# Kernel tuning notes

Measured on AMD Instinct MI355X. Metric: run time of the kernel, lower is better.

The kernel has to match this reference:

```python
import jax, jax.numpy as jnp
import numpy as np
from jax import lax

EPS = 1e-5
NBIT = 127.0  # 8-bit symmetric: 2^(8-1)-1

def ste_round(x):
    return x + lax.stop_gradient(jnp.round(x) - x)

def quant_act(x, rng_max):
    # symmetric fake-quant of activations with learned per-cluster range
    s = rng_max / NBIT
    xq = jnp.clip(ste_round(x / s), -NBIT, NBIT) * s
    return xq, s

def fold_bn(w, gamma, beta, mean, var):
    std = jnp.sqrt(var + EPS)
    scale = gamma / std
    w_f = w * scale[:, None, None, None]
    b_f = beta - mean * scale
    return w_f, b_f

def quant_weight(w):
    # per-output-channel symmetric quant
    s = jnp.max(jnp.abs(w), axis=(1, 2, 3), keepdims=True) / NBIT
    wq = jnp.clip(ste_round(w / s), -NBIT, NBIT) * s
    return wq, s.reshape(-1)

def conv(x, w, stride=1, groups=1, pad=0):
    return lax.conv_general_dilated(
        x, w, window_strides=(stride, stride),
        padding=((pad, pad), (pad, pad)),
        dimension_numbers=('NCHW', 'OIHW', 'NCHW'),
        feature_group_count=groups)

def setup_inputs() -> dict:
    key = jax.random.key(0)
    ks = jax.random.split(key, 24)
    B, Cin, H, W = 64, 96, 28, 28
    Cmid, Cout, NC = 576, 96, 4
    d = {}
    d['x'] = jax.random.normal(ks[0], (B, Cin, H, W), dtype=jnp.float32)
    # conv1: 1x1 expansion
    d['w1'] = jax.random.normal(ks[1], (Cmid, Cin, 1, 1), jnp.float32) * 0.1
    d['g1'] = jax.random.uniform(ks[2], (Cmid,), minval=0.5, maxval=1.5)
    d['b1'] = jax.random.normal(ks[3], (Cmid,)) * 0.1
    d['m1'] = jax.random.normal(ks[4], (Cmid,)) * 0.1
    d['v1'] = jax.random.uniform(ks[5], (Cmid,), minval=0.5, maxval=1.5)
    # conv2: 3x3 depthwise
    d['w2'] = jax.random.normal(ks[6], (Cmid, 1, 3, 3), jnp.float32) * 0.1
    d['g2'] = jax.random.uniform(ks[7], (Cmid,), minval=0.5, maxval=1.5)
    d['b2'] = jax.random.normal(ks[8], (Cmid,)) * 0.1
    d['m2'] = jax.random.normal(ks[9], (Cmid,)) * 0.1
    d['v2'] = jax.random.uniform(ks[10], (Cmid,), minval=0.5, maxval=1.5)
    # conv3: 1x1 projection
    d['w3'] = jax.random.normal(ks[11], (Cout, Cmid, 1, 1), jnp.float32) * 0.1
    d['g3'] = jax.random.uniform(ks[12], (Cout,), minval=0.5, maxval=1.5)
    d['b3'] = jax.random.normal(ks[13], (Cout,)) * 0.1
    d['m3'] = jax.random.normal(ks[14], (Cout,)) * 0.1
    d['v3'] = jax.random.uniform(ks[15], (Cout,), minval=0.5, maxval=1.5)
    # per-cluster learned activation ranges for the 4 QuantAct modules
    d['r0'] = jax.random.uniform(ks[16], (NC,), minval=2.0, maxval=8.0)
    d['r1'] = jax.random.uniform(ks[17], (NC,), minval=2.0, maxval=8.0)
    d['r2'] = jax.random.uniform(ks[18], (NC,), minval=2.0, maxval=8.0)
    d['r3'] = jax.random.uniform(ks[19], (NC,), minval=2.0, maxval=8.0)
    d['cluster'] = 2
    return d

def reference(x, w1, g1, b1, m1, v1, w2, g2, b2, m2, v2,
              w3, g3, b3, m3, v3, r0, r1, r2, r3, cluster):
    identity = x  # residual path (in==out, stride==1)
    # QuantAct -> conv1 (BN-folded, per-channel quant) -> ReLU6
    xq, s0 = quant_act(x, r0[cluster])
    w1f, bf1 = fold_bn(w1, g1, b1, m1, v1)
    w1q, ws1 = quant_weight(w1f)
    y = conv(xq, w1q) + bf1[None, :, None, None]
    y = jnp.clip(y, 0.0, 6.0)
    # QuantAct1 -> depthwise conv2 -> ReLU6
    yq, s1 = quant_act(y, r1[cluster])
    w2f, bf2 = fold_bn(w2, g2, b2, m2, v2)
    w2q, ws2 = quant_weight(w2f)
    y = conv(yq, w2q, stride=1, groups=w2.shape[0], pad=1) + bf2[None, :, None, None]
    y = jnp.clip(y, 0.0, 6.0)
    # QuantAct2 -> conv3 projection
    yq, s2 = quant_act(y, r2[cluster])
    w3f, bf3 = fold_bn(w3, g3, b3, m3, v3)
    w3q, ws3 = quant_weight(w3f)
    y = conv(yq, w3q) + bf3[None, :, None, None]
    # residual add, then int32 requant
    y = y + identity
    out, s3 = quant_act(y, r3[cluster])
    return out, s3
```

## Files before the change

### kernel.cpp

```cpp
#include <hip/hip_runtime.h>
#include <cstdint>
#include <cstddef>

typedef int   v4i __attribute__((ext_vector_type(4)));
typedef float v4f __attribute__((ext_vector_type(4)));
typedef unsigned int u32;

constexpr int B_   = 64;
constexpr int CIN  = 96;
constexpr int P_   = 784;
constexpr int CMID = 576;
constexpr int COUT = 96;
constexpr int NOUT = B_ * COUT * P_;
constexpr float NBITF = 127.0f;
constexpr float EPSF  = 1e-5f;
constexpr float MAGICF = 12582912.0f;
constexpr int   BIASI  = 0x4B400000;

constexpr int XB4 = 13 * 8 * 64;
constexpr int YB4 = 13 * 36 * 64;

__device__ __forceinline__ int dot3(u32 a, u32 w, int acc) {
#if __has_builtin(__builtin_amdgcn_sdot4)
    return __builtin_amdgcn_sdot4((int)a, (int)w, acc, false);
#else
    return acc + (int)(signed char)(a)        * (int)(signed char)(w)
               + (int)(signed char)(a >> 8)   * (int)(signed char)(w >> 8)
               + (int)(signed char)(a >> 16)  * (int)(signed char)(w >> 16);
#endif
}

__device__ __forceinline__ void tr4(u32 S0, u32 S1, u32 S2, u32 S3, u32 O[4]) {
    u32 u01 = __builtin_amdgcn_perm(S1, S0, 0x05010400u);
    u32 u23 = __builtin_amdgcn_perm(S3, S2, 0x05010400u);
    u32 v01 = __builtin_amdgcn_perm(S1, S0, 0x07030602u);
    u32 v23 = __builtin_amdgcn_perm(S3, S2, 0x07030602u);
    O[0] = __builtin_amdgcn_perm(u23, u01, 0x05040100u);
    O[1] = __builtin_amdgcn_perm(u23, u01, 0x07060302u);
    O[2] = __builtin_amdgcn_perm(v23, v01, 0x05040100u);
    O[3] = __builtin_amdgcn_perm(v23, v01, 0x07060302u);
}

__device__ __forceinline__ u32 pack4(u32 t0, u32 t1, u32 t2, u32 t3) {
    u32 p01 = __builtin_amdgcn_perm(t1, t0, 0x05010400u);
    u32 p23 = __builtin_amdgcn_perm(t3, t2, 0x05010400u);
    return __builtin_amdgcn_perm(p23, p01, 0x05040100u);
}

__global__ __launch_bounds__(256)
void prep_all(const float* __restrict__ x,
              const float* __restrict__ w1, const float* __restrict__ g1,
              const float* __restrict__ b1, const float* __restrict__ m1,
              const float* __restrict__ v1,
              const float* __restrict__ w2, const float* __restrict__ g2,
              const float* __restrict__ b2, const float* __restrict__ m2,
              const float* __restrict__ v2,
              const float* __restrict__ w3, const float* __restrict__ g3,
              const float* __restrict__ b3, const float* __restrict__ m3,
              const float* __restrict__ v3,
              const float* __restrict__ r0, const float* __restrict__ r1,
              const float* __restrict__ r2, const int* __restrict__ cluster,
              u32* __restrict__ x8t2,
              int8_t* __restrict__ w1qp, float2* __restrict__ e1,
              v4i* __restrict__ w2pk,    float2* __restrict__ e2,
              int8_t* __restrict__ w3qp, float2* __restrict__ e3)
{
    __shared__ u32 T[112 * 37];
    int tid = threadIdx.x;
    int c = cluster[0];

    if (blockIdx.x < 448) {
        int pt0 = blockIdx.x % 7, b = blockIdx.x / 7;
        float inv_s0 = NBITF / r0[c];

        for (int i = tid; i < 112 * 8; i += 256) {
            int row = i >> 3, cc = 24 + (i & 7);
            T[row * 37 + cc] = 0u;
        }
        for (int u = tid; u < 24 * 28; u += 256) {
            int pq = u % 28, icq = u / 28;
            int pxb = pt0 * 112 + pq * 4;
            int q[4][4];
            #pragma unroll
            for (int j = 0; j < 4; j++) {
                v4f xv = *(const v4f*)(x + ((size_t)b * CIN + icq * 4 + j) * P_ + pxb);
                #pragma unroll
                for (int i = 0; i < 4; i++)
                    q[j][i] = (int)fminf(fmaxf(rintf(xv[i] * inv_s0), -127.f), 127.f);
            }
            #pragma unroll
            for (int i = 0; i < 4; i++) {
                u32 t0 = __builtin_amdgcn_perm((u32)q[1][i], (u32)q[0][i], 0x00000400u);
                u32 t1 = __builtin_amdgcn_perm((u32)q[3][i], (u32)q[2][i], 0x00000400u);
                T[(pq * 4 + i) * 37 + icq] = __builtin_amdgcn_perm(t1, t0, 0x05040100u);
            }
        }
        __syncthreads();
        u32* gb = x8t2 + (size_t)b * XB4 * 4;
        for (int i = tid; i < 32 * 112; i += 256) {
            int icq = i / 112, pxo = i - icq * 112;
            int px = pt0 * 112 + pxo;
            gb[(((px >> 6) * 8 + (icq >> 2)) * 64 + (px & 63)) * 4 + (icq & 3)] =
                T[pxo * 37 + icq];
        }
        return;
    }

    int lane = tid & 63, wv = tid >> 6;
    int blk = (blockIdx.x - 448) * 4 + wv;

    const float *w, *g, *bb, *mm, *vv;
    int oc, K, which;
    if (blk < CMID)            { which = 0; w = w1; g = g1; bb = b1; mm = m1; vv = v1; oc = blk;            K = CIN;  }
    else if (blk < 2 * CMID)   { which = 1; w = w2; g = g2; bb = b2; mm = m2; vv = v2; oc = blk - CMID;     K = 9;    }
    else                       { which = 2; w = w3; g = g3; bb = b3; mm = m3; vv = v3; oc = blk - 2 * CMID; K = CMID; }

    float scale = g[oc] / sqrtf(vv[oc] + EPSF);

    float mx = 0.f;
    for (int k = lane; k < K; k += 64)
        mx = fmaxf(mx, fabsf(w[oc * K + k] * scale));
    #pragma unroll
    for (int off = 1; off < 64; off <<= 1)
        mx = fmaxf(mx, __shfl_xor(mx, off));

    float s = mx / NBITF;

    int myq = 0;
    for (int k = lane; k < K; k += 64) {
        float wf = w[oc * K + k] * scale;
        float q  = fminf(fmaxf(rintf(wf / s), -127.f), 127.f);
        if (which == 0)      w1qp[oc * 144 + k] = (int8_t)q;
        else if (which == 1) myq = (int)q;
        else                 w3qp[oc * 592 + k] = (int8_t)q;
    }
    if (which == 0 && lane < 12)
        ((u32*)(w1qp + oc * 144))[24 + lane] = 0u;
    if (which == 1) {
        u32 qq[9];
        #pragma unroll
        for (int t = 0; t < 9; t++) qq[t] = (u32)__shfl(myq, t, 64) & 0xffu;
        if (lane == 0) {
            v4i pk;
            pk[0] = (int)(qq[0] | (qq[1] << 8) | (qq[2] << 16));
            pk[1] = (int)(qq[3] | (qq[4] << 8) | (qq[5] << 16));
            pk[2] = (int)(qq[6] | (qq[7] << 8) | (qq[8] << 16));
            pk[3] = 0;
            w2pk[oc] = pk;
        }
    }
    if (lane == 0) {
        float bf = bb[oc] - mm[oc] * scale;
        float s0 = r0[c] / NBITF, s1 = r1[c] / NBITF, s2 = r2[c] / NBITF;
        if (which == 0) {
            float inv_s1 = NBITF / r1[c];
            e1[oc] = make_float2(s0 * s * inv_s1, bf * inv_s1);
        } else if (which == 1) {
            float inv_s2 = NBITF / r2[c];
            e2[oc] = make_float2(s1 * s * inv_s2, bf * inv_s2);
        } else {
            e3[oc] = make_float2(s2 * s, bf);
        }
    }
}

__global__ __launch_bounds__(256)
void conv12w(const v4i* __restrict__ x8t2, const v4i* __restrict__ w1q4,
             const float2* __restrict__ e1,
             const v4i* __restrict__ w2pk, const float2* __restrict__ e2,
             const float* __restrict__ r1, const float* __restrict__ r2,
             const int* __restrict__ cluster, v4i* __restrict__ y2t)
{
    __shared__ v4i xs4[8 * 112];
    __shared__ u32 y1w[4][48 * 29];
    __shared__ u32 y2s[4][48 * 15];

    int tid = threadIdx.x, b = blockIdx.y;
    int mt = blockIdx.x / 14, rt = blockIdx.x - mt * 14;
    int R0 = 2 * rt;
    int W0 = (R0 - 1) * 28;
    int lane = tid & 63, wv = tid >> 6;
    int n = lane & 15, q4 = lane >> 4;
    int ocw = mt * 192 + wv * 48;

    int c   = cluster[0];
    int u1i = (int)fminf(rintf(6.f * NBITF / r1[c]), 127.f);
    int u2i = (int)fminf(rintf(6.f * NBITF / r2[c]), 127.f);

    const v4i* xb = x8t2 + (size_t)b * XB4;
    for (int u = tid; u < 896; u += 256) {
        int g = u / 112, pxl = u - g * 112;
        int px = min(max(W0 + pxl, 0), P_ - 1);
        xs4[g * 112 + pxl] = xb[((px >> 6) * 8 + g) * 64 + (px & 63)];
    }
    __syncthreads();

    u32* myY1 = y1w[wv];
    u32* myY2 = y2s[wv];

    v4i    bw[3][2];
    float2 ee[3];
    #pragma unroll
    for (int jn = 0; jn < 3; jn++) {
        int oc = ocw + 16 * jn + n;
        bw[jn][0] = w1q4[oc * 9 + q4];
        bw[jn][1] = w1q4[oc * 9 + 4 + q4];
        ee[jn] = e1[oc];
    }

    #pragma unroll
    for (int jm = 0; jm < 7; jm++) {
        v4i af0 = xs4[q4 * 112 + 16 * jm + n];
        v4i af1 = xs4[(4 + q4) * 112 + 16 * jm + n];

        int dw = 4 * jm + q4;
        bool valid = (unsigned)(W0 + 4 * dw) < (unsigned)P_;

        #pragma unroll
        for (int jn = 0; jn < 3; jn++) {
            v4i acc = (v4i){0, 0, 0, 0};
            acc = __builtin_amdgcn_mfma_i32_16x16x64_i8(af0, bw[jn][0], acc, 0, 0, 0);
            acc = __builtin_amdgcn_mfma_i32_16x16x64_i8(af1, bw[jn][1], acc, 0, 0, 0);

            u32 t[4];
            #pragma unroll
            for (int r = 0; r < 4; r++) {
                float f = fmaf((float)acc[r], ee[jn].x, ee[jn].y) + MAGICF;
                t[r] = (u32)min(max(__float_as_int(f), BIASI), BIASI + u1i);
            }
            u32 pk = pack4(t[0], t[1], t[2], t[3]);
            myY1[(16 * jn + n) * 29 + dw] = valid ? pk : 0u;
        }
    }

    for (int u = lane; u < 96; u += 64) {
        int chl = u >> 1, orow = u & 1;
        int ch  = ocw + chl;
        int rb  = chl * 29 + orow * 7;

        v4i wpk = w2pk[ch];
        u32 pk0 = (u32)wpk[0], pk1 = (u32)wpk[1], pk2 = (u32)wpk[2];
        float2 e = e2[ch];

        u32 M0 = 0, M1 = 0, M2 = 0;
        u32 D0 = myY1[rb], D1 = myY1[rb + 7], D2 = myY1[rb + 14];
        #pragma unroll
        for (int xq = 0; xq < 7; xq++) {
            u32 N0, N1, N2;
            if (xq < 6) {
                N0 = myY1[rb + xq + 1];
                N1 = myY1[rb + 7 + xq + 1];
                N2 = myY1[rb + 14 + xq + 1];
            } else { N0 = N1 = N2 = 0u; }

            int a0, a1, a2, a3;
            a0 = dot3(__builtin_amdgcn_alignbyte(D0, M0, 3), pk0, 0);
            a0 = dot3(__builtin_amdgcn_alignbyte(D1, M1, 3), pk1, a0);
            a0 = dot3(__builtin_amdgcn_alignbyte(D2, M2, 3), pk2, a0);
            a1 = dot3(D0, pk0, 0);
            a1 = dot3(D1, pk1, a1);
            a1 = dot3(D2, pk2, a1);
            a2 = dot3(__builtin_amdgcn_alignbyte(N0, D0, 1), pk0, 0);
            a2 = dot3(__builtin_amdgcn_alignbyte(N1, D1, 1), pk1, a2);
            a2 = dot3(__builtin_amdgcn_alignbyte(N2, D2, 1), pk2, a2);
            a3 = dot3(__builtin_amdgcn_alignbyte(N0, D0, 2), pk0, 0);
            a3 = dot3(__builtin_amdgcn_alignbyte(N1, D1, 2), pk1, a3);
            a3 = dot3(__builtin_amdgcn_alignbyte(N2, D2, 2), pk2, a3);

            int aa[4] = {a0, a1, a2, a3};
            u32 tq[4];
            #pragma unroll
            for (int i = 0; i < 4; i++) {
                float f = fmaf((float)aa[i], e.x, e.y) + MAGICF;
                tq[i] = (u32)min(max(__float_as_int(f), BIASI), BIASI + u2i);
            }
            myY2[chl * 15 + orow * 7 + xq] = pack4(tq[0], tq[1], tq[2], tq[3]);

            M0 = D0; M1 = D1; M2 = D2;
            D0 = N0; D1 = N1; D2 = N2;
        }
    }

    v4i* yb = y2t + (size_t)b * YB4;
    if (lane < 42) {
        int kgl = lane / 14, d = lane - kgl * 14;
        u32 O[4][4];
        #pragma unroll
        for (int j = 0; j < 4; j++) {
            int cb = (16 * kgl + 4 * j) * 15 + d;
            tr4(myY2[cb], myY2[cb + 15], myY2[cb + 30], myY2[cb + 45], O[j]);
        }
        int kgG = mt * 12 + wv * 3 + kgl;
        int gpx0 = R0 * 28 + 4 * d;
        #pragma unroll
        for (int i = 0; i < 4; i++) {
            int gp = gpx0 + i;
            v4i val = (v4i){(int)O[0][i], (int)O[1][i], (int)O[2][i], (int)O[3][i]};
            yb[((gp >> 6) * 36 + kgG) * 64 + (gp & 63)] = val;
        }
    }
}

__global__ __launch_bounds__(256)
void conv3d(const v4i* __restrict__ y2t, const int8_t* __restrict__ w3qp,
            const float2* __restrict__ e3, const float* __restrict__ x,
            const float* __restrict__ r3, const int* __restrict__ cluster,
            float* __restrict__ out)
{
    int tid = threadIdx.x, b = blockIdx.y, pt = blockIdx.x;
    int lane = tid & 63, wv = tid >> 6;
    int n = lane & 15, q4 = lane >> 4;
    int pxl = wv * 16 + n;
    int px  = pt * 64 + pxl;
    int pxc = min(px, P_ - 1);

    int   c      = cluster[0];
    float s3     = r3[c] / NBITF;
    float inv_s3 = NBITF / r3[c];

    const v4i* yb  = y2t + (size_t)b * YB4;
    int pb3 = (pxc >> 6) * (36 * 64) + (pxc & 63);
    const v4i* w34 = (const v4i*)w3qp;

    v4i acc[6];
    #pragma unroll
    for (int i = 0; i < 6; i++) acc[i] = (v4i){0, 0, 0, 0};

    #pragma unroll
    for (int ks = 0; ks < 9; ks++) {
        v4i bfr = yb[pb3 + (4 * ks + q4) * 64];
        #pragma unroll
        for (int i = 0; i < 6; i++) {
            v4i afr = w34[(i * 16 + n) * 37 + 4 * ks + q4];
            acc[i] = __builtin_amdgcn_mfma_i32_16x16x64_i8(afr, bfr, acc[i], 0, 0, 0);
        }
    }

    if (px < P_) {
        #pragma unroll
        for (int i = 0; i < 6; i++) {
            #pragma unroll
            for (int r = 0; r < 4; r++) {
                int    oc = i * 16 + q4 * 4 + r;
                float2 e  = e3[oc];
                size_t gi = (size_t)(b * COUT + oc) * P_ + px;
                float v  = fmaf((float)acc[i][r], e.x, e.y) + x[gi];
                float f  = fmaf(v, inv_s3, MAGICF);
                int lvl  = min(max(__float_as_int(f) - BIASI, -127), 127);
                out[gi]  = (float)lvl * s3;
            }
        }
    }
    if (pt == 0 && b == 0 && tid == 0)
        out[NOUT] = s3;
}

extern "C" void kernel_launch(void* const* d_in, const int* in_sizes, int n_in,
                              void* d_out, int out_size, void* d_ws, size_t ws_size,
                              hipStream_t stream)
{
    const float* x  = (const float*)d_in[0];
    const float* w1 = (const float*)d_in[1];
    const float* g1 = (const float*)d_in[2];
    const float* b1 = (const float*)d_in[3];
    const float* m1 = (const float*)d_in[4];
    const float* v1 = (const float*)d_in[5];
    const float* w2 = (const float*)d_in[6];
    const float* g2 = (const float*)d_in[7];
    const float* b2 = (const float*)d_in[8];
    const float* m2 = (const float*)d_in[9];
    const float* v2 = (const float*)d_in[10];
    const float* w3 = (const float*)d_in[11];
    const float* g3 = (const float*)d_in[12];
    const float* b3 = (const float*)d_in[13];
    const float* m3 = (const float*)d_in[14];
    const float* v3 = (const float*)d_in[15];
    const float* r0 = (const float*)d_in[16];
    const float* r1 = (const float*)d_in[17];
    const float* r2 = (const float*)d_in[18];
    const float* r3 = (const float*)d_in[19];
    const int*   cl = (const int*)d_in[20];

    float* out = (float*)d_out;

    char*  ws  = (char*)d_ws;
    size_t off = 0;
    auto carve = [&](size_t bytes) {
        size_t cur = off;
        off = (off + bytes + 255) & ~(size_t)255;
        return (void*)(ws + cur);
    };
    int8_t* w1qp = (int8_t*)carve((size_t)CMID * 144);
    float2* e1   = (float2*)carve((size_t)CMID * 8);
    v4i*    w2pk = (v4i*)carve((size_t)CMID * 16);
    float2* e2   = (float2*)carve((size_t)CMID * 8);
    int8_t* w3qp = (int8_t*)carve((size_t)COUT * 592);
    float2* e3   = (float2*)carve((size_t)COUT * 8);
    u32*    x8t2 = (u32*)carve((size_t)B_ * XB4 * 16);
    v4i*    y2t  = (v4i*)carve((size_t)B_ * YB4 * 16);
    (void)ws_size; (void)in_sizes; (void)n_in; (void)out_size;

    prep_all<<<dim3(760), dim3(256), 0, stream>>>(
        x, w1, g1, b1, m1, v1, w2, g2, b2, m2, v2, w3, g3, b3, m3, v3,
        r0, r1, r2, cl, x8t2,
        w1qp, e1, w2pk, e2, w3qp, e3);

    conv12w<<<dim3(42, B_), dim3(256), 0, stream>>>(
        (const v4i*)x8t2, (const v4i*)w1qp, e1, w2pk, e2, r1, r2, cl, y2t);

    conv3d<<<dim3(13, B_), dim3(256), 0, stream>>>(
        y2t, w3qp, e3, x, r3, cl, out);
}
```

Before: 169.1 us.

## Fuse projection conv3 into conv12 kernel via shared-memory y2 tile

Merges the depthwise-stage kernel and the projection kernel into a single kernel. Each block now computes all 576 mid channels for a two-row tile, looping over three chunks per wave, and keeps the quantized y2 tile in shared memory for the conv3 MFMA step instead of round-tripping it through a global workspace. This removes the global write and read of the intermediate and one launch. In exchange the grid shrinks to 14x64 blocks with more serial work per block, and the larger shared-memory footprint may lower occupancy.

Result: faster. 164.6 us (-2.6%).

```diff
diff --git a/kernel.cpp b/kernel.cpp
--- a/kernel.cpp
+++ b/kernel.cpp
@@ -18,7 +18,6 @@
 constexpr int   BIASI  = 0x4B400000;
 
 constexpr int XB4 = 13 * 8 * 64;
-constexpr int YB4 = 13 * 36 * 64;
 
 __device__ __forceinline__ int dot3(u32 a, u32 w, int acc) {
 #if __has_builtin(__builtin_amdgcn_sdot4)
@@ -165,27 +164,31 @@
 }
 
 __global__ __launch_bounds__(256)
-void conv12w(const v4i* __restrict__ x8t2, const v4i* __restrict__ w1q4,
+void conv123(const v4i* __restrict__ x8t2, const v4i* __restrict__ w1q4,
              const float2* __restrict__ e1,
              const v4i* __restrict__ w2pk, const float2* __restrict__ e2,
+             const int8_t* __restrict__ w3qp, const float2* __restrict__ e3,
+             const float* __restrict__ x,
              const float* __restrict__ r1, const float* __restrict__ r2,
-             const int* __restrict__ cluster, v4i* __restrict__ y2t)
+             const float* __restrict__ r3, const int* __restrict__ cluster,
+             float* __restrict__ out)
 {
     __shared__ v4i xs4[8 * 112];
-    __shared__ u32 y1w[4][48 * 29];
+    __shared__ u32 y1s[4][48 * 29];
     __shared__ u32 y2s[4][48 * 15];
-
-    int tid = threadIdx.x, b = blockIdx.y;
-    int mt = blockIdx.x / 14, rt = blockIdx.x - mt * 14;
+    __shared__ v4i y2c[36 * 57];
+
+    int tid = threadIdx.x, b = blockIdx.y, rt = blockIdx.x;
     int R0 = 2 * rt;
     int W0 = (R0 - 1) * 28;
     int lane = tid & 63, wv = tid >> 6;
     int n = lane & 15, q4 = lane >> 4;
-    int ocw = mt * 192 + wv * 48;
-
-    int c   = cluster[0];
-    int u1i = (int)fminf(rintf(6.f * NBITF / r1[c]), 127.f);
-    int u2i = (int)fminf(rintf(6.f * NBITF / r2[c]), 127.f);
+
+    int   c      = cluster[0];
+    int   u1i    = (int)fminf(rintf(6.f * NBITF / r1[c]), 127.f);
+    int   u2i    = (int)fminf(rintf(6.f * NBITF / r2[c]), 127.f);
+    float s3     = r3[c] / NBITF;
+    float inv_s3 = NBITF / r3[c];
 
     const v4i* xb = x8t2 + (size_t)b * XB4;
     for (int u = tid; u < 896; u += 256) {
@@ -195,148 +198,129 @@
     }
     __syncthreads();
 
-    u32* myY1 = y1w[wv];
+    u32* myY1 = y1s[wv];
     u32* myY2 = y2s[wv];
 
-    v4i    bw[3][2];
-    float2 ee[3];
+    for (int ck = 0; ck < 3; ck++) {
+        int oc0 = wv * 144 + ck * 48;
+
+        v4i    bw[3][2];
+        float2 ee[3];
+        #pragma unroll
+        for (int jn = 0; jn < 3; jn++) {
+            int oc = oc0 + 16 * jn + n;
+            bw[jn][0] = w1q4[oc * 9 + q4];
+            bw[jn][1] = w1q4[oc * 9 + 4 + q4];
+            ee[jn] = e1[oc];
+        }
+        #pragma unroll
+        for (int jm = 0; jm < 7; jm++) {
+            v4i af0 = xs4[q4 * 112 + 16 * jm + n];
+            v4i af1 = xs4[(4 + q4) * 112 + 16 * jm + n];
+            int dw = 4 * jm + q4;
+            bool valid = (unsigned)(W0 + 4 * dw) < (unsigned)P_;
+
+            #pragma unroll
+            for (int jn = 0; jn < 3; jn++) {
+                v4i acc = (v4i){0, 0, 0, 0};
+                acc = __builtin_amdgcn_mfma_i32_16x16x64_i8(af0, bw[jn][0], acc, 0, 0, 0);
+                acc = __builtin_amdgcn_mfma_i32_16x16x64_i8(af1, bw[jn][1], acc, 0, 0, 0);
+                u32 t[4];
+                #pragma unroll
+                for (int r = 0; r < 4; r++) {
+                    float f = fmaf((float)acc[r], ee[jn].x, ee[jn].y) + MAGICF;
+                    t[r] = (u32)min(max(__float_as_int(f), BIASI), BIASI + u1i);
+                }
+                u32 pk = pack4(t[0], t[1], t[2], t[3]);
+                myY1[(16 * jn + n) * 29 + dw] = valid ? pk : 0u;
+            }
+        }
+
+        for (int u = lane; u < 96; u += 64) {
+            int chl = u >> 1, orow = u & 1;
+            int ch  = oc0 + chl;
+            int rb  = chl * 29 + orow * 7;
+
+            v4i wpk = w2pk[ch];
+            u32 pk0 = (u32)wpk[0], pk1 = (u32)wpk[1], pk2 = (u32)wpk[2];
+            float2 e = e2[ch];
+
+            u32 M0 = 0, M1 = 0, M2 = 0;
+            u32 D0 = myY1[rb], D1 = myY1[rb + 7], D2 = myY1[rb + 14];
+            #pragma unroll
+            for (int xq = 0; xq < 7; xq++) {
+                u32 N0, N1, N2;
+                if (xq < 6) {
+                    N0 = myY1[rb + xq + 1];
+                    N1 = myY1[rb + 7 + xq + 1];
+                    N2 = myY1[rb + 14 + xq + 1];
+                } else { N0 = N1 = N2 = 0u; }
+
+                int a0, a1, a2, a3;
+                a0 = dot3(__builtin_amdgcn_alignbyte(D0, M0, 3), pk0, 0);
+                a0 = dot3(__builtin_amdgcn_alignbyte(D1, M1, 3), pk1, a0);
+                a0 = dot3(__builtin_amdgcn_alignbyte(D2, M2, 3), pk2, a0);
+                a1 = dot3(D0, pk0, 0);
+                a1 = dot3(D1, pk1, a1);
+                a1 = dot3(D2, pk2, a1);
+                a2 = dot3(__builtin_amdgcn_alignbyte(N0, D0, 1), pk0, 0);
+                a2 = dot3(__builtin_amdgcn_alignbyte(N1, D1, 1), pk1, a2);
+                a2 = dot3(__builtin_amdgcn_alignbyte(N2, D2, 1), pk2, a2);
+                a3 = dot3(__builtin_amdgcn_alignbyte(N0, D0, 2), pk0, 0);
+                a3 = dot3(__builtin_amdgcn_alignbyte(N1, D1, 2), pk1, a3);
+                a3 = dot3(__builtin_amdgcn_alignbyte(N2, D2, 2), pk2, a3);
+
+                int aa[4] = {a0, a1, a2, a3};
+                u32 tq[4];
+                #pragma unroll
+                for (int i = 0; i < 4; i++) {
+                    float f = fmaf((float)aa[i], e.x, e.y) + MAGICF;
+                    tq[i] = (u32)min(max(__float_as_int(f), BIASI), BIASI + u2i);
+                }
+                myY2[chl * 15 + orow * 7 + xq] = pack4(tq[0], tq[1], tq[2], tq[3]);
+
+                M0 = D0; M1 = D1; M2 = D2;
+                D0 = N0; D1 = N1; D2 = N2;
+            }
+        }
+
+        if (lane < 42) {
+            int kgl = lane / 14, d = lane - kgl * 14;
+            u32 O[4][4];
+            #pragma unroll
+            for (int j = 0; j < 4; j++) {
+                int cb = (16 * kgl + 4 * j) * 15 + d;
+                tr4(myY2[cb], myY2[cb + 15], myY2[cb + 30], myY2[cb + 45], O[j]);
+            }
+            int kgG = wv * 9 + ck * 3 + kgl;
+            #pragma unroll
+            for (int i = 0; i < 4; i++)
+                y2c[kgG * 57 + 4 * d + i] =
+                    (v4i){(int)O[0][i], (int)O[1][i], (int)O[2][i], (int)O[3][i]};
+        }
+    }
+    __syncthreads();
+
+    int pxl = wv * 16 + n;
+    int pxc = min(pxl, 55);
+    const v4i* w34 = (const v4i*)w3qp;
+
+    v4i acc3[6];
     #pragma unroll
-    for (int jn = 0; jn < 3; jn++) {
-        int oc = ocw + 16 * jn + n;
-        bw[jn][0] = w1q4[oc * 9 + q4];
-        bw[jn][1] = w1q4[oc * 9 + 4 + q4];
-        ee[jn] = e1[oc];
-    }
-
-    #pragma unroll
-    for (int jm = 0; jm < 7; jm++) {
-        v4i af0 = xs4[q4 * 112 + 16 * jm + n];
-        v4i af1 = xs4[(4 + q4) * 112 + 16 * jm + n];
-
-        int dw = 4 * jm + q4;
-        bool valid = (unsigned)(W0 + 4 * dw) < (unsigned)P_;
-
-        #pragma unroll
-        for (int jn = 0; jn < 3; jn++) {
-            v4i acc = (v4i){0, 0, 0, 0};
-            acc = __builtin_amdgcn_mfma_i32_16x16x64_i8(af0, bw[jn][0], acc, 0, 0, 0);
-            acc = __builtin_amdgcn_mfma_i32_16x16x64_i8(af1, bw[jn][1], acc, 0, 0, 0);
-
-            u32 t[4];
-            #pragma unroll
-            for (int r = 0; r < 4; r++) {
-                float f = fmaf((float)acc[r], ee[jn].x, ee[jn].y) + MAGICF;
-                t[r] = (u32)min(max(__float_as_int(f), BIASI), BIASI + u1i);
-            }
-            u32 pk = pack4(t[0], t[1], t[2], t[3]);
-            myY1[(16 * jn + n) * 29 + dw] = valid ? pk : 0u;
-        }
-    }
-
-    for (int u = lane; u < 96; u += 64) {
-        int chl = u >> 1, orow = u & 1;
-        int ch  = ocw + chl;
-        int rb  = chl * 29 + orow * 7;
-
-        v4i wpk = w2pk[ch];
-        u32 pk0 = (u32)wpk[0], pk1 = (u32)wpk[1], pk2 = (u32)wpk[2];
-        float2 e = e2[ch];
-
-        u32 M0 = 0, M1 = 0, M2 = 0;
-        u32 D0 = myY1[rb], D1 = myY1[rb + 7], D2 = myY1[rb + 14];
-        #pragma unroll
-        for (int xq = 0; xq < 7; xq++) {
-            u32 N0, N1, N2;
-            if (xq < 6) {
-                N0 = myY1[rb + xq + 1];
-                N1 = myY1[rb + 7 + xq + 1];
-                N2 = myY1[rb + 14 + xq + 1];
-            } else { N0 = N1 = N2 = 0u; }
-
-            int a0, a1, a2, a3;
-            a0 = dot3(__builtin_amdgcn_alignbyte(D0, M0, 3), pk0, 0);
-            a0 = dot3(__builtin_amdgcn_alignbyte(D1, M1, 3), pk1, a0);
-            a0 = dot3(__builtin_amdgcn_alignbyte(D2, M2, 3), pk2, a0);
-            a1 = dot3(D0, pk0, 0);
-            a1 = dot3(D1, pk1, a1);
-            a1 = dot3(D2, pk2, a1);
-            a2 = dot3(__builtin_amdgcn_alignbyte(N0, D0, 1), pk0, 0);
-            a2 = dot3(__builtin_amdgcn_alignbyte(N1, D1, 1), pk1, a2);
-            a2 = dot3(__builtin_amdgcn_alignbyte(N2, D2, 1), pk2, a2);
-            a3 = dot3(__builtin_amdgcn_alignbyte(N0, D0, 2), pk0, 0);
-            a3 = dot3(__builtin_amdgcn_alignbyte(N1, D1, 2), pk1, a3);
-            a3 = dot3(__builtin_amdgcn_alignbyte(N2, D2, 2), pk2, a3);
-
-            int aa[4] = {a0, a1, a2, a3};
-            u32 tq[4];
-            #pragma unroll
-            for (int i = 0; i < 4; i++) {
-                float f = fmaf((float)aa[i], e.x, e.y) + MAGICF;
-                tq[i] = (u32)min(max(__float_as_int(f), BIASI), BIASI + u2i);
-            }
-            myY2[chl * 15 + orow * 7 + xq] = pack4(tq[0], tq[1], tq[2], tq[3]);
-
-            M0 = D0; M1 = D1; M2 = D2;
-            D0 = N0; D1 = N1; D2 = N2;
-        }
-    }
-
-    v4i* yb = y2t + (size_t)b * YB4;
-    if (lane < 42) {
-        int kgl = lane / 14, d = lane - kgl * 14;
-        u32 O[4][4];
-        #pragma unroll
-        for (int j = 0; j < 4; j++) {
-            int cb = (16 * kgl + 4 * j) * 15 + d;
-            tr4(myY2[cb], myY2[cb + 15], myY2[cb + 30], myY2[cb + 45], O[j]);
-        }
-        int kgG = mt * 12 + wv * 3 + kgl;
-        int gpx0 = R0 * 28 + 4 * d;
-        #pragma unroll
-        for (int i = 0; i < 4; i++) {
-            int gp = gpx0 + i;
-            v4i val = (v4i){(int)O[0][i], (int)O[1][i], (int)O[2][i], (int)O[3][i]};
-            yb[((gp >> 6) * 36 + kgG) * 64 + (gp & 63)] = val;
-        }
-    }
-}
-
-__global__ __launch_bounds__(256)
-void conv3d(const v4i* __restrict__ y2t, const int8_t* __restrict__ w3qp,
-            const float2* __restrict__ e3, const float* __restrict__ x,
-            const float* __restrict__ r3, const int* __restrict__ cluster,
-            float* __restrict__ out)
-{
-    int tid = threadIdx.x, b = blockIdx.y, pt = blockIdx.x;
-    int lane = tid & 63, wv = tid >> 6;
-    int n = lane & 15, q4 = lane >> 4;
-    int pxl = wv * 16 + n;
-    int px  = pt * 64 + pxl;
-    int pxc = min(px, P_ - 1);
-
-    int   c      = cluster[0];
-    float s3     = r3[c] / NBITF;
-    float inv_s3 = NBITF / r3[c];
-
-    const v4i* yb  = y2t + (size_t)b * YB4;
-    int pb3 = (pxc >> 6) * (36 * 64) + (pxc & 63);
-    const v4i* w34 = (const v4i*)w3qp;
-
-    v4i acc[6];
-    #pragma unroll
-    for (int i = 0; i < 6; i++) acc[i] = (v4i){0, 0, 0, 0};
+    for (int i = 0; i < 6; i++) acc3[i] = (v4i){0, 0, 0, 0};
 
     #pragma unroll
     for (int ks = 0; ks < 9; ks++) {
-        v4i bfr = yb[pb3 + (4 * ks + q4) * 64];
+        v4i bfr = y2c[(4 * ks + q4) * 57 + pxc];
         #pragma unroll
         for (int i = 0; i < 6; i++) {
             v4i afr = w34[(i * 16 + n) * 37 + 4 * ks + q4];
-            acc[i] = __builtin_amdgcn_mfma_i32_16x16x64_i8(afr, bfr, acc[i], 0, 0, 0);
-        }
-    }
-
-    if (px < P_) {
+            acc3[i] = __builtin_amdgcn_mfma_i32_16x16x64_i8(afr, bfr, acc3[i], 0, 0, 0);
+        }
+    }
+
+    if (pxl < 56) {
+        int px = R0 * 28 + pxl;
         #pragma unroll
         for (int i = 0; i < 6; i++) {
             #pragma unroll
@@ -344,14 +328,14 @@
                 int    oc = i * 16 + q4 * 4 + r;
                 float2 e  = e3[oc];
                 size_t gi = (size_t)(b * COUT + oc) * P_ + px;
-                float v  = fmaf((float)acc[i][r], e.x, e.y) + x[gi];
+                float v  = fmaf((float)acc3[i][r], e.x, e.y) + x[gi];
                 float f  = fmaf(v, inv_s3, MAGICF);
                 int lvl  = min(max(__float_as_int(f) - BIASI, -127), 127);
                 out[gi]  = (float)lvl * s3;
             }
         }
     }
-    if (pt == 0 && b == 0 && tid == 0)
+    if (rt == 0 && b == 0 && tid == 0)
         out[NOUT] = s3;
 }
 
@@ -397,7 +381,6 @@
     int8_t* w3qp = (int8_t*)carve((size_t)COUT * 592);
     float2* e3   = (float2*)carve((size_t)COUT * 8);
     u32*    x8t2 = (u32*)carve((size_t)B_ * XB4 * 16);
-    v4i*    y2t  = (v4i*)carve((size_t)B_ * YB4 * 16);
     (void)ws_size; (void)in_sizes; (void)n_in; (void)out_size;
 
     prep_all<<<dim3(760), dim3(256), 0, stream>>>(
@@ -405,9 +388,7 @@
         r0, r1, r2, cl, x8t2,
         w1qp, e1, w2pk, e2, w3qp, e3);
 
-    conv12w<<<dim3(42, B_), dim3(256), 0, stream>>>(
-        (const v4i*)x8t2, (const v4i*)w1qp, e1, w2pk, e2, r1, r2, cl, y2t);
-
-    conv3d<<<dim3(13, B_), dim3(256), 0, stream>>>(
-        y2t, w3qp, e3, x, r3, cl, out);
-}
+    conv123<<<dim3(14, B_), dim3(256), 0, stream>>>(
+        (const v4i*)x8t2, (const v4i*)w1qp, e1, w2pk, e2, w3qp, e3,
+        x, r1, r2, r3, cl, out);
+}
```
